# Kernel tuning notes

Measured on AMD Instinct MI355X. Metric: run time of the kernel, lower is better.

Reference implementation:

```python
import jax, jax.numpy as jnp
import numpy as np

EPS = 1e-9
THRESHOLD = 0.2          # second_policy_eval = 'threshold'
CAP_FACTOR = 2.0         # capacity_factor_eval
MIN_EXPERT_CAPACITY = 4


def setup_inputs() -> dict:
    key = jax.random.key(0)
    k1, k2 = jax.random.split(key)
    x = jax.random.normal(k1, (8, 2048, 1024), dtype=jnp.float32)
    W = jax.random.normal(k2, (1024, 64), dtype=jnp.float32) * 0.02
    return {"x": x, "W": W}


def _cumsum_exclusive(t):
    # exclusive cumsum along token dim (-2)
    return jnp.cumsum(t, axis=-2) - t


def reference(x, W):
    b, n, d = x.shape
    e = W.shape[1]
    dt = x.dtype

    raw_gates = jax.nn.softmax(jnp.einsum('bnd,de->bne', x, W), axis=-1)  # [b,n,e]

    gate_1 = jnp.max(raw_gates, axis=-1)            # [b,n]
    index_1 = jnp.argmax(raw_gates, axis=-1)        # [b,n]
    mask_1 = jax.nn.one_hot(index_1, e, dtype=dt)   # [b,n,e]
    density_1_proxy = raw_gates

    gates_wo_top1 = raw_gates * (1.0 - mask_1)
    gate_2 = jnp.max(gates_wo_top1, axis=-1)
    index_2 = jnp.argmax(gates_wo_top1, axis=-1)
    mask_2 = jax.nn.one_hot(index_2, e, dtype=dt)

    denom = gate_1 + gate_2 + EPS
    gate_1 = gate_1 / denom
    gate_2 = gate_2 / denom

    density_1 = jnp.mean(mask_1, axis=-2)                         # [b,e]
    density_1_proxy_m = jnp.mean(density_1_proxy, axis=-2)        # [b,e]
    loss = jnp.mean(density_1_proxy_m * density_1) * float(e ** 2)

    # policy == 'threshold'
    mask_2 = mask_2 * (gate_2 > THRESHOLD).astype(dt)[..., None]

    expert_capacity = max(min(n, int(n * CAP_FACTOR / e)), MIN_EXPERT_CAPACITY)
    cap_f = float(expert_capacity)

    position_in_expert_1 = _cumsum_exclusive(mask_1) * mask_1
    mask_1 = mask_1 * (position_in_expert_1 < cap_f).astype(dt)
    mask_1_count = jnp.sum(mask_1, axis=-2, keepdims=True)        # [b,1,e]
    mask_1_flat = jnp.sum(mask_1, axis=-1)                        # [b,n]
    position_in_expert_1 = jnp.sum(position_in_expert_1, axis=-1) # [b,n]
    gate_1 = gate_1 * mask_1_flat

    position_in_expert_2 = _cumsum_exclusive(mask_2) + mask_1_count
    position_in_expert_2 = position_in_expert_2 * mask_2
    mask_2 = mask_2 * (position_in_expert_2 < cap_f).astype(dt)
    mask_2_flat = jnp.sum(mask_2, axis=-1)
    position_in_expert_2 = jnp.sum(position_in_expert_2, axis=-1)
    gate_2 = gate_2 * mask_2_flat

    # combine: [b, n, e, capacity]
    oh_e1 = jax.nn.one_hot(index_1, e, dtype=dt)[..., None]                                    # [b,n,e,1]
    oh_c1 = jax.nn.one_hot(position_in_expert_1.astype(jnp.int32), expert_capacity, dtype=dt)[..., None, :]  # [b,n,1,cap]
    oh_e2 = jax.nn.one_hot(index_2, e, dtype=dt)[..., None]
    oh_c2 = jax.nn.one_hot(position_in_expert_2.astype(jnp.int32), expert_capacity, dtype=dt)[..., None, :]

    combine_tensor = (
        (gate_1 * mask_1_flat)[..., None, None] * oh_e1 * oh_c1
        + (gate_2 * mask_2_flat)[..., None, None] * oh_e2 * oh_c2
    )
    dispatch_tensor = (combine_tensor != 0).astype(dt)
    return dispatch_tensor, combine_tensor, loss
```

## Files before the change

### kernel.cpp

```cpp
#include <hip/hip_runtime.h>
#include <math.h>

#define BB 8
#define NN 2048
#define DD 1024
#define EE 64
#define CAP 64
#define NTOK (BB * NN)
#define OUT_T_FLOATS 67108864
#define OUT_T_F4     16777216


__global__ __launch_bounds__(1024, 4) void gating_kernel(
    const float* __restrict__ x, const float* __restrict__ W,
    float4* __restrict__ recs, float* __restrict__ dens)
{
    __shared__ float red[4][64][65];
    __shared__ float dred[4][64];

    const int tid  = threadIdx.x;
    const int lane = tid & 63;
    const int wave = __builtin_amdgcn_readfirstlane(tid >> 6);
    const int ks   = wave & 3;
    const int eq   = wave >> 2;
    const int tok  = blockIdx.x * 64 + lane;

    float acc[16];
#pragma unroll
    for (int j = 0; j < 16; ++j) acc[j] = 0.f;

    const float4* xq = (const float4*)(x + (size_t)tok * DD + ks * 256);
    const float*  wq = W + (size_t)(ks * 256) * EE + eq * 16;

#pragma unroll 2
    for (int c = 0; c < 64; ++c) {
        const float4 xv = xq[c];
        const float xs[4] = {xv.x, xv.y, xv.z, xv.w};
#pragma unroll
        for (int kk = 0; kk < 4; ++kk) {
            const float4* wr = (const float4*)(wq + (size_t)(c * 4 + kk) * EE);
            const float4 w0 = wr[0], w1 = wr[1], w2 = wr[2], w3 = wr[3];
            acc[ 0] = fmaf(xs[kk], w0.x, acc[ 0]);
            acc[ 1] = fmaf(xs[kk], w0.y, acc[ 1]);
            acc[ 2] = fmaf(xs[kk], w0.z, acc[ 2]);
            acc[ 3] = fmaf(xs[kk], w0.w, acc[ 3]);
            acc[ 4] = fmaf(xs[kk], w1.x, acc[ 4]);
            acc[ 5] = fmaf(xs[kk], w1.y, acc[ 5]);
            acc[ 6] = fmaf(xs[kk], w1.z, acc[ 6]);
            acc[ 7] = fmaf(xs[kk], w1.w, acc[ 7]);
            acc[ 8] = fmaf(xs[kk], w2.x, acc[ 8]);
            acc[ 9] = fmaf(xs[kk], w2.y, acc[ 9]);
            acc[10] = fmaf(xs[kk], w2.z, acc[10]);
            acc[11] = fmaf(xs[kk], w2.w, acc[11]);
            acc[12] = fmaf(xs[kk], w3.x, acc[12]);
            acc[13] = fmaf(xs[kk], w3.y, acc[13]);
            acc[14] = fmaf(xs[kk], w3.z, acc[14]);
            acc[15] = fmaf(xs[kk], w3.w, acc[15]);
        }
    }

#pragma unroll
    for (int j = 0; j < 16; ++j)
        red[ks][eq * 16 + j][lane] = acc[j];
    __syncthreads();

    if (wave < 4) {
        const int t0 = wave * 16;
        float densacc = 0.f;
#pragma unroll 1
        for (int ti = 0; ti < 16; ++ti) {
            const int t = t0 + ti;
            const float lv = ((red[0][lane][t] + red[1][lane][t])
                            + red[2][lane][t]) + red[3][lane][t];

            float v = lv; int bi = lane;
#pragma unroll
            for (int off = 32; off; off >>= 1) {
                float ov = __shfl_xor(v, off);
                int   oi = __shfl_xor(bi, off);
                if (ov > v || (ov == v && oi < bi)) { v = ov; bi = oi; }
            }
            const float m1 = v; const int i1 = bi;
            float v2 = (lane == i1) ? -INFINITY : lv; int b2 = lane;
#pragma unroll
            for (int off = 32; off; off >>= 1) {
                float ov = __shfl_xor(v2, off);
                int   oi = __shfl_xor(b2, off);
                if (ov > v2 || (ov == v2 && oi < b2)) { v2 = ov; b2 = oi; }
            }
            const float m2 = v2; const int i2 = b2;

            float ex = expf(lv - m1);
            float Z = ex;
#pragma unroll
            for (int off = 32; off; off >>= 1) Z += __shfl_xor(Z, off);
            float g1 = 1.0f / Z;
            float g2 = expf(m2 - m1) * g1;
            float den = g1 + g2 + 1e-9f;
            float g1n = g1 / den;
            float g2n = g2 / den;
            int flag = (g2n > 0.2f) ? 1 : 0;

            densacc += ex * g1;

            if (lane == 0)
                recs[blockIdx.x * 64 + t] =
                    make_float4(g1n, g2n, __int_as_float(i1),
                                __int_as_float(i2 | (flag << 8)));
        }
        dred[wave][lane] = densacc;
    }
    __syncthreads();
    if (tid < 64) {
        float s = dred[0][tid] + dred[1][tid] + dred[2][tid] + dred[3][tid];
        dens[blockIdx.x * 64 + tid] = s;
    }
}

__global__ __launch_bounds__(1024) void scan_kernel(
    const float4* __restrict__ recs, const float* __restrict__ dens,
    float4* __restrict__ frecs, float* __restrict__ lossp)
{
    const int b = blockIdx.x;
    __shared__ int hist1[32][64], pre1[32][64];
    __shared__ int hist2[32][64], pre2[32][64];
    __shared__ int base2[64];
    __shared__ float dsum[64];

    const int tid = threadIdx.x;
    const int lane = tid & 63;
    const int wave = tid >> 6;

    float4 r[2];
    int e1[2], e2[2], fl[2], rank1[2], rank2[2];
    const unsigned long long below = (1ull << lane) - 1ull;

#pragma unroll
    for (int u = 0; u < 2; ++u) {
        const int g = 2 * wave + u;
        const int tok = g * 64 + lane;
        float4 rr = recs[b * NN + tok];
        r[u] = rr;
        e1[u] = __float_as_int(rr.z);
        int i2f = __float_as_int(rr.w);
        e2[u] = i2f & 63;
        fl[u] = i2f >> 8;

        unsigned long long m = ~0ull, mv = ~0ull;
#pragma unroll
        for (int bit = 0; bit < 6; ++bit) {
            unsigned long long vt = __ballot((e1[u] >> bit) & 1);
            m  &= ((e1[u] >> bit) & 1) ? vt : ~vt;
            mv &= ((lane  >> bit) & 1) ? vt : ~vt;
        }
        rank1[u] = __popcll(m & below);
        hist1[g][lane] = __popcll(mv);

        unsigned long long fv = __ballot(fl[u]);
        m = fv; mv = fv;
#pragma unroll
        for (int bit = 0; bit < 6; ++bit) {
            unsigned long long vt = __ballot((e2[u] >> bit) & 1);
            m  &= ((e2[u] >> bit) & 1) ? vt : ~vt;
            mv &= ((lane  >> bit) & 1) ? vt : ~vt;
        }
        rank2[u] = __popcll(m & below);
        hist2[g][lane] = __popcll(mv);
    }

    if (wave == 0) {
        float s = 0.f;
        for (int k = 0; k < 32; ++k) s += dens[(b * 32 + k) * 64 + lane];
        dsum[lane] = s;
    }
    __syncthreads();

    if (wave == 0) {
        int run = 0;
#pragma unroll
        for (int g = 0; g < 32; ++g) { pre1[g][lane] = run; run += hist1[g][lane]; }
        base2[lane] = run < CAP ? run : CAP;
        int run2 = 0;
#pragma unroll
        for (int g = 0; g < 32; ++g) { pre2[g][lane] = run2; run2 += hist2[g][lane]; }
        float v = dsum[lane] * (float)run;
#pragma unroll
        for (int off = 32; off; off >>= 1) v += __shfl_xor(v, off);
        if (lane == 0) lossp[b] = v;
    }
    __syncthreads();

#pragma unroll
    for (int u = 0; u < 2; ++u) {
        const int g = 2 * wave + u;
        const int tok = g * 64 + lane;
        int p1 = rank1[u] + pre1[g][e1[u]];
        int k1 = p1 < CAP;
        int p2 = rank2[u] + pre2[g][e2[u]] + base2[e2[u]];
        int k2 = fl[u] && (p2 < CAP);
        float4 fr;
        fr.x = k1 ? r[u].x : 0.f;
        fr.y = k2 ? r[u].y : 0.f;
        fr.z = __int_as_float(k1 ? (e1[u] * CAP + p1) : -1);
        fr.w = __int_as_float(k2 ? (e2[u] * CAP + p2) : -1);
        frecs[b * NN + tok] = fr;
    }
}

__global__ __launch_bounds__(256) void fill_kernel(
    const float4* __restrict__ frecs, const float* __restrict__ lossp,
    float* __restrict__ out)
{
    const int tid = blockIdx.x * 256 + threadIdx.x;
    const int token = tid >> 10;
    const int e  = (tid >> 4) & 63;
    const int c4 = tid & 15;
    float4 r = frecs[token];

    float cx = 0.f, cy = 0.f, cz = 0.f, cw = 0.f;
    float dx = 0.f, dy = 0.f, dz = 0.f, dw = 0.f;

    int p1 = __float_as_int(r.z);
    if (p1 >= 0 && (p1 >> 6) == e && ((p1 >> 2) & 15) == c4) {
        int cc = p1 & 3;
        if      (cc == 0) { cx = r.x; dx = 1.f; }
        else if (cc == 1) { cy = r.x; dy = 1.f; }
        else if (cc == 2) { cz = r.x; dz = 1.f; }
        else              { cw = r.x; dw = 1.f; }
    }
    int p2 = __float_as_int(r.w);
    if (p2 >= 0 && (p2 >> 6) == e && ((p2 >> 2) & 15) == c4) {
        int cc = p2 & 3;
        if      (cc == 0) { cx = r.y; dx = 1.f; }
        else if (cc == 1) { cy = r.y; dy = 1.f; }
        else if (cc == 2) { cz = r.y; dz = 1.f; }
        else              { cw = r.y; dw = 1.f; }
    }

    float4* o4 = (float4*)out;
    o4[tid]             = make_float4(dx, dy, dz, dw);
    o4[tid + OUT_T_F4]  = make_float4(cx, cy, cz, cw);

    if (tid == 0) {
        float s = 0.f;
        for (int k = 0; k < 8; ++k) s += lossp[k];
        out[2 * (size_t)OUT_T_FLOATS] = s * (1.0f / 524288.0f);
    }
}

extern "C" void kernel_launch(void* const* d_in, const int* in_sizes, int n_in,
                              void* d_out, int out_size, void* d_ws, size_t ws_size,
                              hipStream_t stream)
{
    const float* x = (const float*)d_in[0];
    const float* W = (const float*)d_in[1];
    float* out = (float*)d_out;
    char* ws = (char*)d_ws;

    float4* recs  = (float4*)(ws);
    float4* frecs = (float4*)(ws + 262144);
    float*  dens  = (float*)(ws + 524288);
    float*  lossp = (float*)(ws + 589824);

    gating_kernel<<<256, 1024, 0, stream>>>(x, W, recs, dens);
    scan_kernel<<<8, 1024, 0, stream>>>(recs, dens, frecs, lossp);
    fill_kernel<<<65536, 256, 0, stream>>>(frecs, lossp, out);
}
```

Measured before the change: 612.3 us.

## Stage x tiles in LDS with double buffering and drop the split-K reduction

```diff
diff --git a/kernel.cpp b/kernel.cpp
--- a/kernel.cpp
+++ b/kernel.cpp
@@ -15,53 +15,48 @@
     const float* __restrict__ x, const float* __restrict__ W,
     float4* __restrict__ recs, float* __restrict__ dens)
 {
-    __shared__ float red[4][64][65];
+    __shared__ float xl[2][64][68];
+    __shared__ float logits[64][65];
     __shared__ float dred[4][64];
 
     const int tid  = threadIdx.x;
     const int lane = tid & 63;
     const int wave = __builtin_amdgcn_readfirstlane(tid >> 6);
-    const int ks   = wave & 3;
-    const int eq   = wave >> 2;
-    const int tok  = blockIdx.x * 64 + lane;
-
-    float acc[16];
-#pragma unroll
-    for (int j = 0; j < 16; ++j) acc[j] = 0.f;
-
-    const float4* xq = (const float4*)(x + (size_t)tok * DD + ks * 256);
-    const float*  wq = W + (size_t)(ks * 256) * EE + eq * 16;
-
-#pragma unroll 2
-    for (int c = 0; c < 64; ++c) {
-        const float4 xv = xq[c];
-        const float xs[4] = {xv.x, xv.y, xv.z, xv.w};
-#pragma unroll
-        for (int kk = 0; kk < 4; ++kk) {
-            const float4* wr = (const float4*)(wq + (size_t)(c * 4 + kk) * EE);
-            const float4 w0 = wr[0], w1 = wr[1], w2 = wr[2], w3 = wr[3];
-            acc[ 0] = fmaf(xs[kk], w0.x, acc[ 0]);
-            acc[ 1] = fmaf(xs[kk], w0.y, acc[ 1]);
-            acc[ 2] = fmaf(xs[kk], w0.z, acc[ 2]);
-            acc[ 3] = fmaf(xs[kk], w0.w, acc[ 3]);
-            acc[ 4] = fmaf(xs[kk], w1.x, acc[ 4]);
-            acc[ 5] = fmaf(xs[kk], w1.y, acc[ 5]);
-            acc[ 6] = fmaf(xs[kk], w1.z, acc[ 6]);
-            acc[ 7] = fmaf(xs[kk], w1.w, acc[ 7]);
-            acc[ 8] = fmaf(xs[kk], w2.x, acc[ 8]);
-            acc[ 9] = fmaf(xs[kk], w2.y, acc[ 9]);
-            acc[10] = fmaf(xs[kk], w2.z, acc[10]);
-            acc[11] = fmaf(xs[kk], w2.w, acc[11]);
-            acc[12] = fmaf(xs[kk], w3.x, acc[12]);
-            acc[13] = fmaf(xs[kk], w3.y, acc[13]);
-            acc[14] = fmaf(xs[kk], w3.z, acc[14]);
-            acc[15] = fmaf(xs[kk], w3.w, acc[15]);
-        }
-    }
-
-#pragma unroll
-    for (int j = 0; j < 16; ++j)
-        red[ks][eq * 16 + j][lane] = acc[j];
+    const int tok0 = blockIdx.x * 64;
+
+    const int srow = tid >> 4;
+    const int scol = tid & 15;
+    const float4* xsrc = (const float4*)(x + (size_t)(tok0 + srow) * DD) + scol;
+
+    const float* wbase = W + wave * 4;
+
+    float acc[4] = {0.f, 0.f, 0.f, 0.f};
+    float4 pre = xsrc[0];
+
+#pragma unroll 1
+    for (int c = 0; c < 16; ++c) {
+        *(float4*)&xl[c & 1][srow][scol * 4] = pre;
+        if (c < 15) pre = xsrc[(c + 1) * 16];
+        __syncthreads();
+#pragma unroll
+        for (int c4 = 0; c4 < 16; ++c4) {
+            const float4 xv = *(const float4*)&xl[c & 1][lane][c4 * 4];
+            const float xs[4] = {xv.x, xv.y, xv.z, xv.w};
+#pragma unroll
+            for (int kk = 0; kk < 4; ++kk) {
+                const int k = c * 64 + c4 * 4 + kk;
+                const float4 wv = *(const float4*)(wbase + (size_t)k * EE);
+                acc[0] = fmaf(xs[kk], wv.x, acc[0]);
+                acc[1] = fmaf(xs[kk], wv.y, acc[1]);
+                acc[2] = fmaf(xs[kk], wv.z, acc[2]);
+                acc[3] = fmaf(xs[kk], wv.w, acc[3]);
+            }
+        }
+    }
+
+#pragma unroll
+    for (int j = 0; j < 4; ++j)
+        logits[lane][wave * 4 + j] = acc[j];
     __syncthreads();
 
     if (wave < 4) {
@@ -70,8 +65,7 @@
 #pragma unroll 1
         for (int ti = 0; ti < 16; ++ti) {
             const int t = t0 + ti;
-            const float lv = ((red[0][lane][t] + red[1][lane][t])
-                            + red[2][lane][t]) + red[3][lane][t];
+            const float lv = logits[t][lane];
 
             float v = lv; int bi = lane;
 #pragma unroll
```

After: 664.6 us. 1.09x slower.
